# Performance work log

Measured on AMD Instinct MI355X. Metric: run time of the kernel, lower is better.

## Reference

```python
import jax, jax.numpy as jnp
import numpy as np

# Dimensions (Llama-3-8B-style GQA with paged KV cache)
B, S, HID = 1, 1024, 4096
H, HKV, D = 32, 8, 128
G = H // HKV
BLK = 16            # tokens per KV block
NB = 256            # blocks in storage
CB = 192            # context blocks attended (3072 tokens)
PAST = 2048         # tokens already cached before this step
NL = 2              # layers in kv_ptr
L = CB * BLK


def rotate_half(x):
    x1, x2 = x[..., : x.shape[-1] // 2], x[..., x.shape[-1] // 2:]
    return jnp.concatenate([-x2, x1], axis=-1)


def setup_inputs() -> dict:
    key = jax.random.key(0)
    ks = jax.random.split(key, 8)
    hidden_states = jax.random.normal(ks[0], (B, S, HID), jnp.float32)
    kv_ptr = jax.random.normal(ks[1], (NL, 2, NB, HKV, BLK, D), jnp.float32)
    Wq = 0.02 * jax.random.normal(ks[2], (H * D, HID), jnp.float32)
    Wk = 0.02 * jax.random.normal(ks[3], (HKV * D, HID), jnp.float32)
    Wv = 0.02 * jax.random.normal(ks[4], (HKV * D, HID), jnp.float32)
    Wo = 0.02 * jax.random.normal(ks[5], (HID, H * D), jnp.float32)
    # RoPE cache for the new tokens (global positions PAST..PAST+S-1), HF convention
    pos = (PAST + jnp.arange(S)).astype(jnp.float32)
    inv_freq = 1.0 / (10000.0 ** (jnp.arange(0, D, 2, dtype=jnp.float32) / D))
    freqs = pos[:, None] * inv_freq[None, :]                # [S, D/2]
    emb = jnp.concatenate([freqs, freqs], axis=-1)           # [S, D]
    cos = jnp.cos(emb)[None, None]                           # [1,1,S,D]
    sin = jnp.sin(emb)[None, None]
    new_q_lut = jnp.arange(S, dtype=jnp.int32)[None]         # identity query LUT
    new_kv_lut = (CB - S // BLK + jnp.arange(S // BLK, dtype=jnp.int32))[None]  # blocks 128..191
    all_kv_lut = jnp.arange(CB, dtype=jnp.int32)[None]       # blocks 0..191
    kv_pos = jnp.arange(L)
    q_pos = PAST + jnp.arange(S)
    mask = (kv_pos[None, None, :] <= q_pos[None, :, None])   # [1,S,L] causal over global positions
    cmd_groups = jnp.zeros((B, S), jnp.int32)                # split-K scheduling metadata (no math effect)
    return dict(hidden_states=hidden_states, kv_ptr=kv_ptr, new_q_lut=new_q_lut,
                new_kv_lut=new_kv_lut, all_kv_lut=all_kv_lut, mask=mask,
                cmd_groups=cmd_groups, cos=cos, sin=sin, Wq=Wq, Wk=Wk, Wv=Wv, Wo=Wo,
                layer_idx=0)


def reference(hidden_states, kv_ptr, new_q_lut, new_kv_lut, all_kv_lut, mask,
              cmd_groups, cos, sin, Wq, Wk, Wv, Wo, layer_idx):
    b, s, _ = hidden_states.shape
    # QKV projections (no bias)
    q = jnp.einsum('bsh,oh->bso', hidden_states, Wq).reshape(b, s, H, D).transpose(0, 2, 1, 3)
    k = jnp.einsum('bsh,oh->bso', hidden_states, Wk).reshape(b, s, HKV, D).transpose(0, 2, 1, 3)
    v = jnp.einsum('bsh,oh->bso', hidden_states, Wv).reshape(b, s, HKV, D).transpose(0, 2, 1, 3)
    # RoPE
    q = q * cos + rotate_half(q) * sin
    k = k * cos + rotate_half(k) * sin
    # fill_kv_block_storage: scatter new K/V blocks into this layer's storage (b == 1)
    kb = jnp.transpose(k[0].reshape(HKV, s // BLK, BLK, D), (1, 0, 2, 3))  # [nblk,HKV,BLK,D]
    vb = jnp.transpose(v[0].reshape(HKV, s // BLK, BLK, D), (1, 0, 2, 3))
    sk = kv_ptr[layer_idx, 0].at[new_kv_lut[0]].set(kb)
    sv = kv_ptr[layer_idx, 1].at[new_kv_lut[0]].set(vb)
    # qkv_attention: gather context blocks via LUT, masked GQA attention
    ck = jnp.transpose(sk[all_kv_lut[0]], (1, 0, 2, 3)).reshape(HKV, L, D)  # [HKV,L,D]
    cv = jnp.transpose(sv[all_kv_lut[0]], (1, 0, 2, 3)).reshape(HKV, L, D)
    qg = q[:, :, new_q_lut[0], :].reshape(b, HKV, G, s, D)
    scores = jnp.einsum('bkgsd,kld->bkgsl', qg, ck) / jnp.sqrt(jnp.float32(D))
    scores = jnp.where(mask[:, None, None], scores, jnp.finfo(scores.dtype).min)
    p = jax.nn.softmax(scores, axis=-1)
    o = jnp.einsum('bkgsl,kld->bkgsd', p, cv).reshape(b, H, s, D)
    o = o.transpose(0, 2, 1, 3).reshape(b, s, H * D)
    return jnp.einsum('bso,ho->bsh', o, Wo)
```

## Files before the change

kernel.cpp:

```cpp
#include <hip/hip_runtime.h>
#include <cstdint>
#include <cstddef>


typedef _Float16 f16;
typedef f16 f16x8 __attribute__((ext_vector_type(8)));
typedef f16 f16x4 __attribute__((ext_vector_type(4)));
typedef float f32x4 __attribute__((ext_vector_type(4)));

#define HIDN 4096
#define LCTX 3072
#define PASTN 2048
#define QK_SCALE_LOG2 0.12753102734366334f
#define RESC_THR 11.54f

__device__ __forceinline__ f32x4 mfma16(f16x8 a, f16x8 b, f32x4 c) {
    return __builtin_amdgcn_mfma_f32_16x16x32_f16(a, b, c, 0, 0, 0);
}
__device__ __forceinline__ f32x4 mfma16k16(f16x4 a, f16x4 b, f32x4 c) {
    return __builtin_amdgcn_mfma_f32_16x16x16f16(a, b, c, 0, 0, 0);
}

__device__ __forceinline__ void gl_lds16(const void* g, void* l) {
    auto gp = (const __attribute__((address_space(1))) unsigned int*)(uintptr_t)g;
    auto lp = (__attribute__((address_space(3))) unsigned int*)(uintptr_t)l;
    __builtin_amdgcn_global_load_lds(gp, lp, 16, 0, 0);
}

__device__ __forceinline__ uint32_t lds_lo(const void* p) {
    return (uint32_t)(uintptr_t)p;
}

#define TRRD(dst, va, OFF) \
    asm volatile("ds_read_b64_tr_b16 %0, %1 offset:" #OFF : "=v"(dst) : "v"(va))
#define WAITL(N) \
    asm volatile("s_waitcnt lgkmcnt(" #N ")" ::: "memory"); \
    __builtin_amdgcn_sched_barrier(0)

__global__ void cvt_all(const float* __restrict__ hidden, const float* __restrict__ Wq,
                        const float* __restrict__ Wk, const float* __restrict__ Wv,
                        f16* __restrict__ h16, f16* __restrict__ w16)
{
    int i = blockIdx.x * 256 + threadIdx.x;
    const float* src; f16* dst; int off;
    if (i < 1048576)      { src = hidden; dst = h16; off = i; }
    else if (i < 5242880) { src = Wq; dst = w16; off = i - 1048576; }
    else if (i < 6291456) { src = Wk; dst = w16 + (size_t)4096 * 4096; off = i - 5242880; }
    else                  { src = Wv; dst = w16 + (size_t)5120 * 4096; off = i - 6291456; }
    f32x4 v = *(const f32x4*)(src + (size_t)off * 4);
    f16x4 h;
#pragma unroll
    for (int j = 0; j < 4; j++) h[j] = (f16)v[j];
    *(f16x4*)(dst + (size_t)off * 4) = h;
}

template <int EPI, int BM>
__global__ __launch_bounds__(256, 3) void gemm_f16(
    const f16* __restrict__ A, const f16* __restrict__ B,
    float* __restrict__ Cf, f16* __restrict__ Cq, f16* __restrict__ Ck,
    f16* __restrict__ Cv, int M, int N, int K,
    const float* __restrict__ kvp, const int* __restrict__ layer,
    f16* __restrict__ ckc)
{
    __shared__ f16 As[BM * 64];
    __shared__ f16 Bs[128 * 64];

    const int bx = blockIdx.x;

    if (EPI == 0 && bx >= 384) {
        const int lay = layer[0];
        int base = (bx - 384) * 256 + threadIdx.x;
#pragma unroll
        for (int pass = 0; pass < 32; ++pass) {
            int i4 = base + pass * 32768;
            int half = i4 >> 19;
            int e = (i4 & 524287) * 4;
            int hh = e >> 18, rem = e & 262143, l = rem >> 7, d = rem & 127;
            int blk = l >> 4, rr = l & 15;
            size_t src = (((size_t)(lay * 2 + half) * 256 + blk) * 8 + hh) * 2048
                       + (size_t)rr * 128 + d;
            f32x4 x = *(const f32x4*)(kvp + src);
            f16x4 h;
#pragma unroll
            for (int j = 0; j < 4; j++) h[j] = (f16)x[j];
            size_t dst = ((size_t)hh * LCTX + l) * 128 + d;
            *(f16x4*)((half ? Cv : ckc) + dst) = h;
        }
        return;
    }

    constexpr int RPW = BM / 4;
    constexpr int MI  = BM / 32;

    const int t = threadIdx.x, lane = t & 63, w = t >> 6;
    const int wm = w >> 1, wn = w & 1;
    const int l16 = lane & 15, g16 = lane >> 4;
    const int nx = (EPI == 0) ? 48 : 32;
    const int m0 = (bx / nx) * BM, n0 = (bx % nx) * 128;

    const int srow = lane >> 3;
    const int sgr  = (lane & 7) ^ srow;

    const size_t aoff = (size_t)(m0 + w * RPW + srow) * K + sgr * 8;
    const size_t boff = (size_t)(n0 + w * 32 + srow) * K + sgr * 8;

    f32x4 acc[MI][4];
#pragma unroll
    for (int i = 0; i < MI; i++)
#pragma unroll
        for (int j = 0; j < 4; j++) acc[i][j] = (f32x4){0.f, 0.f, 0.f, 0.f};

    for (int k0 = 0; k0 < K; k0 += 64) {
#pragma unroll
        for (int j = 0; j < RPW / 8; j++)
            gl_lds16(A + aoff + (size_t)j * 8 * K + k0,
                     (void*)(As + (w * RPW + j * 8) * 64));
#pragma unroll
        for (int j = 0; j < 4; j++)
            gl_lds16(B + boff + (size_t)j * 8 * K + k0,
                     (void*)(Bs + (w * 32 + j * 8) * 64));
        __syncthreads();

#pragma unroll
        for (int ks = 0; ks < 2; ks++) {
            f16x8 af[MI], bfr[4];
#pragma unroll
            for (int mi = 0; mi < MI; mi++) {
                int r = wm * (BM / 2) + mi * 16 + l16;
                int g = ks * 4 + g16;
                af[mi] = *(const f16x8*)&As[r * 64 + ((g ^ (r & 7)) << 3)];
            }
#pragma unroll
            for (int ni = 0; ni < 4; ni++) {
                int r = wn * 64 + ni * 16 + l16;
                int g = ks * 4 + g16;
                bfr[ni] = *(const f16x8*)&Bs[r * 64 + ((g ^ (r & 7)) << 3)];
            }
#pragma unroll
            for (int ni = 0; ni < 4; ni++)
#pragma unroll
                for (int mi = 0; mi < MI; mi++)
                    acc[mi][ni] = mfma16(af[mi], bfr[ni], acc[mi][ni]);
        }
        __syncthreads();
    }

#pragma unroll
    for (int mi = 0; mi < MI; mi++)
#pragma unroll
        for (int ni = 0; ni < 4; ni++)
#pragma unroll
            for (int r = 0; r < 4; r++) {
                int row = m0 + wm * (BM / 2) + mi * 16 + (g16 << 2) + r;
                int col = n0 + wn * 64 + ni * 16 + l16;
                float val = acc[mi][ni][r];
                if (EPI == 0) {
                    if (col < 4096) {
                        Cq[(size_t)row * 4096 + col] = (f16)val;
                    } else if (col < 5120) {
                        Ck[(size_t)row * 1024 + (col - 4096)] = (f16)val;
                    } else {
                        int c = col - 5120;
                        int hh = c >> 7, d = c & 127;
                        Cv[((size_t)hh * LCTX + PASTN + row) * 128 + d] = (f16)val;
                    }
                } else {
                    Cf[(size_t)row * N + col] = val;
                }
            }
}

__global__ void aux2(const float* __restrict__ Wo, f16* __restrict__ w16,
                     f16* __restrict__ q16, const f16* __restrict__ kraw,
                     const float* __restrict__ cosp, const float* __restrict__ sinp,
                     f16* __restrict__ ck)
{
    int i = blockIdx.x * 256 + threadIdx.x;
    if (i < 4194304) {
        f32x4 v = *(const f32x4*)(Wo + (size_t)i * 4);
        f16x4 h;
#pragma unroll
        for (int j = 0; j < 4; j++) h[j] = (f16)v[j];
        *(f16x4*)(w16 + (size_t)i * 4) = h;
    } else if (i < 4456448) {
        int ii = i - 4194304;
        int gd = ii & 7, hh = (ii >> 3) & 31, s = ii >> 8;
        size_t b1 = (size_t)s * 4096 + hh * 128 + gd * 8;
        f16x8 x1 = *(f16x8*)(q16 + b1);
        f16x8 x2 = *(f16x8*)(q16 + b1 + 64);
        const float* c1 = cosp + s * 128 + gd * 8;
        const float* s1 = sinp + s * 128 + gd * 8;
        f16x8 o1, o2;
#pragma unroll
        for (int j = 0; j < 8; j++) {
            float a = (float)x1[j], b = (float)x2[j];
            o1[j] = (f16)((a * c1[j] - b * s1[j]) * QK_SCALE_LOG2);
            o2[j] = (f16)((b * c1[j + 64] + a * s1[j + 64]) * QK_SCALE_LOG2);
        }
        *(f16x8*)(q16 + b1) = o1;
        *(f16x8*)(q16 + b1 + 64) = o2;
    } else {
        int ii = i - 4456448;
        int gd = ii & 7, kvh = (ii >> 3) & 7, s = ii >> 6;
        size_t b1 = (size_t)s * 1024 + kvh * 128 + gd * 8;
        f16x8 x1 = *(const f16x8*)(kraw + b1);
        f16x8 x2 = *(const f16x8*)(kraw + b1 + 64);
        const float* c1 = cosp + s * 128 + gd * 8;
        const float* s1 = sinp + s * 128 + gd * 8;
        f16x8 o1, o2;
#pragma unroll
        for (int j = 0; j < 8; j++) {
            float a = (float)x1[j], b = (float)x2[j];
            o1[j] = (f16)(a * c1[j] - b * s1[j]);
            o2[j] = (f16)(b * c1[j + 64] + a * s1[j + 64]);
        }
        size_t dst = ((size_t)kvh * LCTX + PASTN + s) * 128 + gd * 8;
        *(f16x8*)(ck + dst) = o1;
        *(f16x8*)(ck + dst + 64) = o2;
    }
}

__global__ __launch_bounds__(256, 2) void attn_part(
    const f16* __restrict__ Q, const f16* __restrict__ Kc,
    const f16* __restrict__ Vc, f16* __restrict__ Op, float* __restrict__ mlb)
{
    const int b = blockIdx.x;
    const int z = b >> 8;
    const int idx = b & 255;
    const int h = idx & 31;
    const int jj = idx >> 5;
    const int j = z ? (7 - jj) : jj;
    const int s0 = j * 128;
    const int kvh = h >> 2;
    const int t = threadIdx.x, lane = t & 63, w = t >> 6;
    const int l16 = lane & 15, g16 = lane >> 4;

    __shared__ f16 Ks[2][64 * 128];
    __shared__ f16 Vs[2][64 * 128];

    f16x8 qfA[4], qfB[4];
    {
        size_t baseA = (size_t)(s0 + w * 32 + l16) * 4096 + h * 128;
        size_t baseB = baseA + (size_t)16 * 4096;
#pragma unroll
        for (int kk = 0; kk < 4; kk++) {
            qfA[kk] = *(const f16x8*)(Q + baseA + kk * 32 + g16 * 8);
            qfB[kk] = *(const f16x8*)(Q + baseB + kk * 32 + g16 * 8);
        }
    }

    f32x4 ofA[8], ofB[8];
#pragma unroll
    for (int cf = 0; cf < 8; cf++) {
        ofA[cf] = (f32x4){0.f, 0.f, 0.f, 0.f};
        ofB[cf] = (f32x4){0.f, 0.f, 0.f, 0.f};
    }
    float mrA = -3.0e38f, lrA = 0.f;
    float mrB = -3.0e38f, lrB = 0.f;

    const f16* Kb = Kc + (size_t)kvh * LCTX * 128;
    const f16* Vb = Vc + (size_t)kvh * LCTX * 128;
    const int ntt = (PASTN + s0 + 128) >> 6;

    const int krow = lane >> 4;
    const int kp   = lane & 15;
    const int vrow = ((lane >> 5) << 4) + (((lane >> 3) & 3) << 2) + ((lane >> 1) & 3);
    const int vch  = (lane & 1) << 3;

    const uint32_t vs0 = lds_lo(Vs[0]) + lane * 8;
    const uint32_t vs1 = lds_lo(Vs[1]) + lane * 8;

#define STAGE_KV(l0, buf)                                                     \
    {                                                                         \
        _Pragma("unroll")                                                     \
        for (int jx = 0; jx < 4; jx++) {                                      \
            int r7 = ((jx & 1) << 2) + krow;                                  \
            int sg = kp ^ r7;                                                 \
            gl_lds16(Kb + (size_t)((l0) + w * 16 + jx * 4 + krow) * 128 + sg * 8, \
                     (void*)(Ks[buf] + (w * 16 + jx * 4) * 128));             \
        }                                                                     \
        _Pragma("unroll")                                                     \
        for (int q = 0; q < 4; q++) {                                         \
            gl_lds16(Vb + (size_t)((l0) + (q & 1) * 32 + vrow) * 128          \
                        + (w * 2 + (q >> 1)) * 16 + vch,                      \
                     (void*)(Vs[buf] + (w * 4 + q) * 512));                   \
        }                                                                     \
    }

    STAGE_KV(z * 64, 0);
    __syncthreads();

    int itp = 0;
    for (int it = z; it < ntt; it += 2, ++itp) {
        const int l0 = it << 6;
        const int cur = itp & 1;

        if (it + 2 < ntt) STAGE_KV(l0 + 128, cur ^ 1);

        f32x4 sA[4], sB[4];
#pragma unroll
        for (int ni = 0; ni < 4; ni++) {
            sA[ni] = (f32x4){0.f, 0.f, 0.f, 0.f};
            sB[ni] = (f32x4){0.f, 0.f, 0.f, 0.f};
        }
        __builtin_amdgcn_s_setprio(1);
#pragma unroll
        for (int ni = 0; ni < 4; ni++)
#pragma unroll
            for (int kk = 0; kk < 4; kk++) {
                int r = ni * 16 + l16;
                int g = kk * 4 + g16;
                f16x8 kh = *(const f16x8*)&Ks[cur][r * 128 + ((g ^ (r & 7)) << 3)];
                sA[ni] = mfma16(kh, qfA[kk], sA[ni]);
                sB[ni] = mfma16(kh, qfB[kk], sB[ni]);
            }
        __builtin_amdgcn_s_setprio(0);

#define SOFTMAX(sf, mr, lr, of, QOFF)                                          \
        {                                                                      \
            const int qrow = s0 + w * 32 + (QOFF) + l16;                       \
            if (l0 + 63 > PASTN + s0 + w * 32 + (QOFF)) {                      \
                _Pragma("unroll")                                              \
                for (int ni = 0; ni < 4; ni++)                                 \
                    _Pragma("unroll")                                          \
                    for (int r = 0; r < 4; r++) {                              \
                        int col = l0 + ni * 16 + (g16 << 2) + r;               \
                        if (col > PASTN + qrow) sf[ni][r] = -3.0e38f;          \
                    }                                                          \
            }                                                                  \
            float mx;                                                          \
            {                                                                  \
                f32x4 m4 = sf[0];                                              \
                _Pragma("unroll")                                              \
                for (int ni = 1; ni < 4; ni++) {                               \
                    m4[0] = fmaxf(m4[0], sf[ni][0]);                           \
                    m4[1] = fmaxf(m4[1], sf[ni][1]);                           \
                    m4[2] = fmaxf(m4[2], sf[ni][2]);                           \
                    m4[3] = fmaxf(m4[3], sf[ni][3]);                           \
                }                                                              \
                mx = fmaxf(fmaxf(m4[0], m4[1]), fmaxf(m4[2], m4[3]));          \
            }                                                                  \
            mx = fmaxf(mx, __shfl_xor(mx, 16));                                \
            mx = fmaxf(mx, __shfl_xor(mx, 32));                                \
            if (__any(mx > mr + RESC_THR)) {                                   \
                float mnew = fmaxf(mr, mx);                                    \
                float corr = exp2f(mr - mnew);                                 \
                mr = mnew;                                                     \
                lr *= corr;                                                    \
                float cr[4];                                                   \
                _Pragma("unroll")                                              \
                for (int r = 0; r < 4; r++) cr[r] = __shfl(corr, (g16 << 2) + r); \
                _Pragma("unroll")                                              \
                for (int cf = 0; cf < 8; cf++)                                 \
                    _Pragma("unroll")                                          \
                    for (int r = 0; r < 4; r++) of[cf][r] *= cr[r];            \
            }                                                                  \
            _Pragma("unroll")                                                  \
            for (int ni = 0; ni < 4; ni++)                                     \
                _Pragma("unroll")                                              \
                for (int r = 0; r < 4; r++) {                                  \
                    float p = exp2f(sf[ni][r] - mr);                           \
                    sf[ni][r] = p;                                             \
                    lr += p;                                                   \
                }                                                              \
        }

        SOFTMAX(sA, mrA, lrA, ofA, 0)
        SOFTMAX(sB, mrB, lrB, ofB, 16)

        f16x4 paA[4], paB[4];
#pragma unroll
        for (int ni = 0; ni < 4; ni++) {
            paA[ni][0] = (f16)sA[ni][0]; paA[ni][1] = (f16)sA[ni][1];
            paA[ni][2] = (f16)sA[ni][2]; paA[ni][3] = (f16)sA[ni][3];
            paB[ni][0] = (f16)sB[ni][0]; paB[ni][1] = (f16)sB[ni][1];
            paB[ni][2] = (f16)sB[ni][2]; paB[ni][3] = (f16)sB[ni][3];
        }

        {
            const uint32_t va = cur ? vs1 : vs0;
            f16x4 ra0, ra1, ra2, ra3, rb0, rb1, rb2, rb3;
            f16x4 rc0, rc1, rc2, rc3, rd0, rd1, rd2, rd3;
            __builtin_amdgcn_s_setprio(1);
            TRRD(ra0,va,0);     TRRD(ra1,va,512);   TRRD(ra2,va,1024);  TRRD(ra3,va,1536);
            TRRD(rb0,va,2048);  TRRD(rb1,va,2560);  TRRD(rb2,va,3072);  TRRD(rb3,va,3584);
            TRRD(rc0,va,4096);  TRRD(rc1,va,4608);  TRRD(rc2,va,5120);  TRRD(rc3,va,5632);
#define X2(cf, ni, reg) \
            ofA[cf] = mfma16k16(paA[ni], reg, ofA[cf]); \
            ofB[cf] = mfma16k16(paB[ni], reg, ofB[cf]);
            WAITL(8);
            X2(0,0,ra0) X2(0,1,ra1) X2(0,2,ra2) X2(0,3,ra3)
            TRRD(rd0,va,6144);  TRRD(rd1,va,6656);  TRRD(rd2,va,7168);  TRRD(rd3,va,7680);
            WAITL(8);
            X2(1,0,rb0) X2(1,1,rb1) X2(1,2,rb2) X2(1,3,rb3)
            TRRD(ra0,va,8192);  TRRD(ra1,va,8704);  TRRD(ra2,va,9216);  TRRD(ra3,va,9728);
            WAITL(8);
            X2(2,0,rc0) X2(2,1,rc1) X2(2,2,rc2) X2(2,3,rc3)
            TRRD(rb0,va,10240); TRRD(rb1,va,10752); TRRD(rb2,va,11264); TRRD(rb3,va,11776);
            WAITL(8);
            X2(3,0,rd0) X2(3,1,rd1) X2(3,2,rd2) X2(3,3,rd3)
            TRRD(rc0,va,12288); TRRD(rc1,va,12800); TRRD(rc2,va,13312); TRRD(rc3,va,13824);
            WAITL(8);
            X2(4,0,ra0) X2(4,1,ra1) X2(4,2,ra2) X2(4,3,ra3)
            TRRD(rd0,va,14336); TRRD(rd1,va,14848); TRRD(rd2,va,15360); TRRD(rd3,va,15872);
            WAITL(8);
            X2(5,0,rb0) X2(5,1,rb1) X2(5,2,rb2) X2(5,3,rb3)
            WAITL(4);
            X2(6,0,rc0) X2(6,1,rc1) X2(6,2,rc2) X2(6,3,rc3)
            WAITL(0);
            X2(7,0,rd0) X2(7,1,rd1) X2(7,2,rd2) X2(7,3,rd3)
#undef X2
            __builtin_amdgcn_s_setprio(0);
        }
        __syncthreads();
    }

#define WRITE_P(of, mr, lr, QOFF)                                             \
    {                                                                         \
        float l2 = lr + __shfl_xor(lr, 16);                                   \
        l2 += __shfl_xor(l2, 32);                                             \
        if (lane < 16) {                                                      \
            int srow = s0 + w * 32 + (QOFF) + lane;                           \
            *(float2*)(mlb + (((size_t)z * 1024 + srow) * 32 + h) * 2) =      \
                make_float2(mr, l2);                                          \
        }                                                                     \
        float lrr[4];                                                         \
        _Pragma("unroll")                                                     \
        for (int r = 0; r < 4; r++) lrr[r] = __shfl(l2, (g16 << 2) + r);      \
        _Pragma("unroll")                                                     \
        for (int cf = 0; cf < 8; cf++)                                        \
            _Pragma("unroll")                                                 \
            for (int r = 0; r < 4; r++) {                                     \
                int srow = s0 + w * 32 + (QOFF) + (g16 << 2) + r;             \
                int d = cf * 16 + l16;                                        \
                Op[(size_t)z * 4194304 + (size_t)srow * 4096                  \
                   + (size_t)h * 128 + d] = (f16)(of[cf][r] / lrr[r]);        \
            }                                                                 \
    }
    WRITE_P(ofA, mrA, lrA, 0)
    WRITE_P(ofB, mrB, lrB, 16)
#undef WRITE_P
#undef SOFTMAX
#undef STAGE_KV
}

__global__ void attn_combine(const f16* __restrict__ Op, const float* __restrict__ mlb,
                             f16* __restrict__ obuf)
{
    int i = blockIdx.x * 256 + threadIdx.x;
    int d8 = i & 15, hh = (i >> 4) & 31, s = i >> 9;
    float2 ml0 = *(const float2*)(mlb + (((size_t)0 * 1024 + s) * 32 + hh) * 2);
    float2 ml1 = *(const float2*)(mlb + (((size_t)1 * 1024 + s) * 32 + hh) * 2);
    float mstar = fmaxf(ml0.x, ml1.x);
    float w0 = exp2f(ml0.x - mstar) * ml0.y;
    float w1 = exp2f(ml1.x - mstar) * ml1.y;
    float inv = 1.0f / (w0 + w1);
    size_t off = (size_t)s * 4096 + (size_t)hh * 128 + d8 * 8;
    f16x8 a = *(const f16x8*)(Op + off);
    f16x8 b = *(const f16x8*)(Op + 4194304 + off);
    f16x8 o;
#pragma unroll
    for (int jx = 0; jx < 8; jx++)
        o[jx] = (f16)(((float)a[jx] * w0 + (float)b[jx] * w1) * inv);
    *(f16x8*)(obuf + off) = o;
}

extern "C" void kernel_launch(void* const* d_in, const int* in_sizes, int n_in,
                              void* d_out, int out_size, void* d_ws, size_t ws_size,
                              hipStream_t stream)
{
    const float* hidden = (const float*)d_in[0];
    const float* kvp    = (const float*)d_in[1];
    const float* cosp   = (const float*)d_in[7];
    const float* sinp   = (const float*)d_in[8];
    const float* Wq     = (const float*)d_in[9];
    const float* Wk     = (const float*)d_in[10];
    const float* Wv     = (const float*)d_in[11];
    const float* Wo     = (const float*)d_in[12];
    const int*   layer  = (const int*)d_in[13];

    char* ws = (char*)d_ws;
    f16* w16  = (f16*)ws;
    f16* opart= (f16*)(ws + 33554432);
    f16* h16  = (f16*)(ws + 50331648);
    f16* ck   = (f16*)(ws + 58720256);
    f16* cv   = (f16*)(ws + 65011712);
    f16* obuf = (f16*)(ws + 71303168);

    f16*   q16  = (f16*)d_out;
    f16*   kraw = (f16*)((char*)d_out + 8388608);
    float* mlb  = (float*)((char*)d_out + 8388608);

    cvt_all<<<28672, 256, 0, stream>>>(hidden, Wq, Wk, Wv, h16, w16);

    gemm_f16<0, 128><<<dim3(512), 256, 0, stream>>>(
        h16, w16, nullptr, q16, kraw, cv, 1024, 6144, 4096, kvp, layer, ck);

    aux2<<<17664, 256, 0, stream>>>(Wo, w16, q16, kraw, cosp, sinp, ck);

    attn_part<<<dim3(512), 256, 0, stream>>>(q16, ck, cv, opart, mlb);

    attn_combine<<<2048, 256, 0, stream>>>(opart, mlb, obuf);

    gemm_f16<1, 64><<<dim3(512), 256, 0, stream>>>(
        obuf, w16, (float*)d_out, nullptr, nullptr, nullptr, 1024, 4096, 4096,
        nullptr, nullptr, nullptr);
}
```

Measured before the change: 274.0 us.

## Split attention KV range four ways instead of two and combine four partials

The attention kernel now launches 1024 blocks, with each block handling every fourth 64-token KV tile instead of every second. Partial outputs go to four separate workspace buffers and the combine step merges four (m, l) pairs. It also precomputes the staging offsets and advances pointers incrementally instead of recomputing addresses each tile. The goal is more parallelism and better CU occupancy. The cost is more partial-output traffic and a heavier combine, and one partial buffer reuses the h16 region, which relies on h16 no longer being needed.

```diff
diff --git a/kernel.cpp b/kernel.cpp
--- a/kernel.cpp
+++ b/kernel.cpp
@@ -222,14 +222,15 @@
 
 __global__ __launch_bounds__(256, 2) void attn_part(
     const f16* __restrict__ Q, const f16* __restrict__ Kc,
-    const f16* __restrict__ Vc, f16* __restrict__ Op, float* __restrict__ mlb)
+    const f16* __restrict__ Vc, f16* __restrict__ Op0, f16* __restrict__ Op1,
+    f16* __restrict__ Op2, f16* __restrict__ Op3, float* __restrict__ mlb)
 {
     const int b = blockIdx.x;
     const int z = b >> 8;
     const int idx = b & 255;
     const int h = idx & 31;
     const int jj = idx >> 5;
-    const int j = z ? (7 - jj) : jj;
+    const int j = (z & 1) ? (7 - jj) : jj;
     const int s0 = j * 128;
     const int kvh = h >> 2;
     const int t = threadIdx.x, lane = t & 63, w = t >> 6;
@@ -238,6 +239,8 @@
     __shared__ f16 Ks[2][64 * 128];
     __shared__ f16 Vs[2][64 * 128];
 
+    f16* Op = (z == 0) ? Op0 : (z == 1) ? Op1 : (z == 2) ? Op2 : Op3;
+
     f16x8 qfA[4], qfB[4];
     {
         size_t baseA = (size_t)(s0 + w * 32 + l16) * 4096 + h * 128;
@@ -258,8 +261,6 @@
     float mrA = -3.0e38f, lrA = 0.f;
     float mrB = -3.0e38f, lrB = 0.f;
 
-    const f16* Kb = Kc + (size_t)kvh * LCTX * 128;
-    const f16* Vb = Vc + (size_t)kvh * LCTX * 128;
     const int ntt = (PASTN + s0 + 128) >> 6;
 
     const int krow = lane >> 4;
@@ -267,35 +268,42 @@
     const int vrow = ((lane >> 5) << 4) + (((lane >> 3) & 3) << 2) + ((lane >> 1) & 3);
     const int vch  = (lane & 1) << 3;
 
+    int koff[4], vof[4], kd[4], vd[4];
+#pragma unroll
+    for (int jx = 0; jx < 4; jx++) {
+        int r7 = ((jx & 1) << 2) + krow;
+        koff[jx] = (w * 16 + jx * 4 + krow) * 128 + ((kp ^ r7) << 3);
+        kd[jx]   = (w * 16 + jx * 4) * 128;
+        vof[jx]  = ((jx & 1) * 32 + vrow) * 128 + (w * 2 + (jx >> 1)) * 16 + vch;
+        vd[jx]   = (w * 4 + jx) * 512;
+    }
+    const f16* kptr = Kc + (size_t)kvh * LCTX * 128 + (size_t)(z * 64) * 128;
+    const f16* vptr = Vc + (size_t)kvh * LCTX * 128 + (size_t)(z * 64) * 128;
+
     const uint32_t vs0 = lds_lo(Vs[0]) + lane * 8;
     const uint32_t vs1 = lds_lo(Vs[1]) + lane * 8;
 
-#define STAGE_KV(l0, buf)                                                     \
+#define STAGE_KV(buf)                                                         \
     {                                                                         \
         _Pragma("unroll")                                                     \
-        for (int jx = 0; jx < 4; jx++) {                                      \
-            int r7 = ((jx & 1) << 2) + krow;                                  \
-            int sg = kp ^ r7;                                                 \
-            gl_lds16(Kb + (size_t)((l0) + w * 16 + jx * 4 + krow) * 128 + sg * 8, \
-                     (void*)(Ks[buf] + (w * 16 + jx * 4) * 128));             \
-        }                                                                     \
+        for (int jx = 0; jx < 4; jx++)                                        \
+            gl_lds16(kptr + koff[jx], (void*)(Ks[buf] + kd[jx]));             \
         _Pragma("unroll")                                                     \
-        for (int q = 0; q < 4; q++) {                                         \
-            gl_lds16(Vb + (size_t)((l0) + (q & 1) * 32 + vrow) * 128          \
-                        + (w * 2 + (q >> 1)) * 16 + vch,                      \
-                     (void*)(Vs[buf] + (w * 4 + q) * 512));                   \
-        }                                                                     \
-    }
-
-    STAGE_KV(z * 64, 0);
+        for (int jx = 0; jx < 4; jx++)                                        \
+            gl_lds16(vptr + vof[jx], (void*)(Vs[buf] + vd[jx]));              \
+        kptr += 4 * 64 * 128;                                                 \
+        vptr += 4 * 64 * 128;                                                 \
+    }
+
+    STAGE_KV(0);
     __syncthreads();
 
     int itp = 0;
-    for (int it = z; it < ntt; it += 2, ++itp) {
+    for (int it = z; it < ntt; it += 4, ++itp) {
         const int l0 = it << 6;
         const int cur = itp & 1;
 
-        if (it + 2 < ntt) STAGE_KV(l0 + 128, cur ^ 1);
+        if (it + 4 < ntt) STAGE_KV(cur ^ 1);
 
         f32x4 sA[4], sB[4];
 #pragma unroll
@@ -433,8 +441,8 @@
             for (int r = 0; r < 4; r++) {                                     \
                 int srow = s0 + w * 32 + (QOFF) + (g16 << 2) + r;             \
                 int d = cf * 16 + l16;                                        \
-                Op[(size_t)z * 4194304 + (size_t)srow * 4096                  \
-                   + (size_t)h * 128 + d] = (f16)(of[cf][r] / lrr[r]);        \
+                Op[(size_t)srow * 4096 + (size_t)h * 128 + d] =               \
+                    (f16)(of[cf][r] / lrr[r]);                                \
             }                                                                 \
     }
     WRITE_P(ofA, mrA, lrA, 0)
@@ -444,25 +452,34 @@
 #undef STAGE_KV
 }
 
-__global__ void attn_combine(const f16* __restrict__ Op, const float* __restrict__ mlb,
-                             f16* __restrict__ obuf)
+__global__ void attn_combine(f16* Op0, const f16* Op1, const f16* Op2,
+                             const f16* Op3, const float* mlb)
 {
     int i = blockIdx.x * 256 + threadIdx.x;
     int d8 = i & 15, hh = (i >> 4) & 31, s = i >> 9;
-    float2 ml0 = *(const float2*)(mlb + (((size_t)0 * 1024 + s) * 32 + hh) * 2);
-    float2 ml1 = *(const float2*)(mlb + (((size_t)1 * 1024 + s) * 32 + hh) * 2);
-    float mstar = fmaxf(ml0.x, ml1.x);
-    float w0 = exp2f(ml0.x - mstar) * ml0.y;
-    float w1 = exp2f(ml1.x - mstar) * ml1.y;
-    float inv = 1.0f / (w0 + w1);
+    float m[4], l[4];
+#pragma unroll
+    for (int zz = 0; zz < 4; zz++) {
+        float2 ml = *(const float2*)(mlb + (((size_t)zz * 1024 + s) * 32 + hh) * 2);
+        m[zz] = ml.x; l[zz] = ml.y;
+    }
+    float mstar = fmaxf(fmaxf(m[0], m[1]), fmaxf(m[2], m[3]));
+    float wt[4];
+    float tot = 0.f;
+#pragma unroll
+    for (int zz = 0; zz < 4; zz++) { wt[zz] = exp2f(m[zz] - mstar) * l[zz]; tot += wt[zz]; }
+    float inv = 1.0f / tot;
     size_t off = (size_t)s * 4096 + (size_t)hh * 128 + d8 * 8;
-    f16x8 a = *(const f16x8*)(Op + off);
-    f16x8 b = *(const f16x8*)(Op + 4194304 + off);
+    f16x8 a0 = *(const f16x8*)(Op0 + off);
+    f16x8 a1 = *(const f16x8*)(Op1 + off);
+    f16x8 a2 = *(const f16x8*)(Op2 + off);
+    f16x8 a3 = *(const f16x8*)(Op3 + off);
     f16x8 o;
 #pragma unroll
     for (int jx = 0; jx < 8; jx++)
-        o[jx] = (f16)(((float)a[jx] * w0 + (float)b[jx] * w1) * inv);
-    *(f16x8*)(obuf + off) = o;
+        o[jx] = (f16)(((float)a0[jx] * wt[0] + (float)a1[jx] * wt[1]
+                     + (float)a2[jx] * wt[2] + (float)a3[jx] * wt[3]) * inv);
+    *(f16x8*)(Op0 + off) = o;
 }
 
 extern "C" void kernel_launch(void* const* d_in, const int* in_sizes, int n_in,
@@ -480,12 +497,14 @@
     const int*   layer  = (const int*)d_in[13];
 
     char* ws = (char*)d_ws;
-    f16* w16  = (f16*)ws;
-    f16* opart= (f16*)(ws + 33554432);
-    f16* h16  = (f16*)(ws + 50331648);
-    f16* ck   = (f16*)(ws + 58720256);
-    f16* cv   = (f16*)(ws + 65011712);
-    f16* obuf = (f16*)(ws + 71303168);
+    f16* w16    = (f16*)ws;
+    f16* opart0 = (f16*)(ws + 33554432);
+    f16* opart1 = (f16*)(ws + 41943040);
+    f16* h16    = (f16*)(ws + 50331648);
+    f16* opart2 = (f16*)(ws + 50331648);
+    f16* ck     = (f16*)(ws + 58720256);
+    f16* cv     = (f16*)(ws + 65011712);
+    f16* opart3 = (f16*)(ws + 71303168);
 
     f16*   q16  = (f16*)d_out;
     f16*   kraw = (f16*)((char*)d_out + 8388608);
@@ -498,11 +517,12 @@
 
     aux2<<<17664, 256, 0, stream>>>(Wo, w16, q16, kraw, cosp, sinp, ck);
 
-    attn_part<<<dim3(512), 256, 0, stream>>>(q16, ck, cv, opart, mlb);
-
-    attn_combine<<<2048, 256, 0, stream>>>(opart, mlb, obuf);
+    attn_part<<<dim3(1024), 256, 0, stream>>>(
+        q16, ck, cv, opart0, opart1, opart2, opart3, mlb);
+
+    attn_combine<<<2048, 256, 0, stream>>>(opart0, opart1, opart2, opart3, mlb);
 
     gemm_f16<1, 64><<<dim3(512), 256, 0, stream>>>(
-        obuf, w16, (float*)d_out, nullptr, nullptr, nullptr, 1024, 4096, 4096,
+        opart0, w16, (float*)d_out, nullptr, nullptr, nullptr, 1024, 4096, 4096,
         nullptr, nullptr, nullptr);
 }
```

After: 277.5 us. About the same (+1.3%).

## Move Wo fp16 conversion into tail of light attention blocks

Applied to the files above, without the earlier changes.

Takes the Wo fp32-to-fp16 conversion out of the aux2 kernel and appends it to the end of attention blocks that process early query tiles. Those blocks have less causal work, so the conversion can fill their idle time while heavier blocks are still running. The 64 MB read and 32 MB write of Wo then overlap with attention instead of running as a separate serial phase. The risk is extra register pressure or a longer tail in attn_part if the light blocks are not actually idle.

```diff
diff --git a/kernel.cpp b/kernel.cpp
--- a/kernel.cpp
+++ b/kernel.cpp
@@ -170,21 +170,13 @@
             }
 }
 
-__global__ void aux2(const float* __restrict__ Wo, f16* __restrict__ w16,
-                     f16* __restrict__ q16, const f16* __restrict__ kraw,
+__global__ void aux2(f16* __restrict__ q16, const f16* __restrict__ kraw,
                      const float* __restrict__ cosp, const float* __restrict__ sinp,
                      f16* __restrict__ ck)
 {
     int i = blockIdx.x * 256 + threadIdx.x;
-    if (i < 4194304) {
-        f32x4 v = *(const f32x4*)(Wo + (size_t)i * 4);
-        f16x4 h;
-#pragma unroll
-        for (int j = 0; j < 4; j++) h[j] = (f16)v[j];
-        *(f16x4*)(w16 + (size_t)i * 4) = h;
-    } else if (i < 4456448) {
-        int ii = i - 4194304;
-        int gd = ii & 7, hh = (ii >> 3) & 31, s = ii >> 8;
+    if (i < 262144) {
+        int gd = i & 7, hh = (i >> 3) & 31, s = i >> 8;
         size_t b1 = (size_t)s * 4096 + hh * 128 + gd * 8;
         f16x8 x1 = *(f16x8*)(q16 + b1);
         f16x8 x2 = *(f16x8*)(q16 + b1 + 64);
@@ -200,7 +192,7 @@
         *(f16x8*)(q16 + b1) = o1;
         *(f16x8*)(q16 + b1 + 64) = o2;
     } else {
-        int ii = i - 4456448;
+        int ii = i - 262144;
         int gd = ii & 7, kvh = (ii >> 3) & 7, s = ii >> 6;
         size_t b1 = (size_t)s * 1024 + kvh * 128 + gd * 8;
         f16x8 x1 = *(const f16x8*)(kraw + b1);
@@ -222,7 +214,8 @@
 
 __global__ __launch_bounds__(256, 2) void attn_part(
     const f16* __restrict__ Q, const f16* __restrict__ Kc,
-    const f16* __restrict__ Vc, f16* __restrict__ Op, float* __restrict__ mlb)
+    const f16* __restrict__ Vc, f16* __restrict__ Op, float* __restrict__ mlb,
+    const float* __restrict__ Wo, f16* __restrict__ w16)
 {
     const int b = blockIdx.x;
     const int z = b >> 8;
@@ -442,6 +435,22 @@
 #undef WRITE_P
 #undef SOFTMAX
 #undef STAGE_KV
+
+    if (j < 4) {
+        int js  = z ? (jj - 4) : jj;
+        int cid = h * 8 + js * 2 + z;
+        const float* src = Wo + (size_t)cid * 65536;
+        f16* dst = w16 + (size_t)cid * 65536;
+#pragma unroll 4
+        for (int p = 0; p < 64; ++p) {
+            int e = (p * 256 + t) * 4;
+            f32x4 v = *(const f32x4*)(src + e);
+            f16x4 hv;
+#pragma unroll
+            for (int jx = 0; jx < 4; jx++) hv[jx] = (f16)v[jx];
+            *(f16x4*)(dst + e) = hv;
+        }
+    }
 }
 
 __global__ void attn_combine(const f16* __restrict__ Op, const float* __restrict__ mlb,
@@ -496,9 +505,9 @@
     gemm_f16<0, 128><<<dim3(512), 256, 0, stream>>>(
         h16, w16, nullptr, q16, kraw, cv, 1024, 6144, 4096, kvp, layer, ck);
 
-    aux2<<<17664, 256, 0, stream>>>(Wo, w16, q16, kraw, cosp, sinp, ck);
-
-    attn_part<<<dim3(512), 256, 0, stream>>>(q16, ck, cv, opart, mlb);
+    aux2<<<1280, 256, 0, stream>>>(q16, kraw, cosp, sinp, ck);
+
+    attn_part<<<dim3(512), 256, 0, stream>>>(q16, ck, cv, opart, mlb, Wo, w16);
 
     attn_combine<<<2048, 256, 0, stream>>>(opart, mlb, obuf);
 
```

Measured after the change: 264.5 us. 1.04x faster.
